# Kernel tuning notes

Measured on AMD Instinct MI355X. Metric: run time of the kernel, lower is better.

Reference implementation:

```python
import jax, jax.numpy as jnp
import numpy as np

B, S, D, H = 2, 2048, 1024, 16
HD = D // H

def setup_inputs() -> dict:
    key = jax.random.key(0)
    ks = jax.random.split(key, 11)
    s = 1.0 / np.sqrt(D)
    return {
        "query": jax.random.normal(ks[0], (B, S, D), jnp.float32),
        "key": jax.random.normal(ks[1], (B, S, D), jnp.float32),
        "value": jax.random.normal(ks[2], (B, S, D), jnp.float32),
        "Wq": jax.random.normal(ks[3], (D, D), jnp.float32) * s,
        "bq": jax.random.normal(ks[4], (D,), jnp.float32) * s,
        "Wk": jax.random.normal(ks[5], (D, D), jnp.float32) * s,
        "bk": jax.random.normal(ks[6], (D,), jnp.float32) * s,
        "Wv": jax.random.normal(ks[7], (D, D), jnp.float32) * s,
        "bv": jax.random.normal(ks[8], (D,), jnp.float32) * s,
        "Wo": jax.random.normal(ks[9], (D, D), jnp.float32) * s,
        "bo": jax.random.normal(ks[10], (D,), jnp.float32) * s,
        "test": 0,
    }

def _heads(x, W, b):
    # [B,S,D] @ [D,D] -> [B,S,D] -> [B,H,S,HD]
    y = x @ W + b
    return y.reshape(B, -1, H, HD).transpose(0, 2, 1, 3)

def reference(query, key, value, Wq, bq, Wk, bk, Wv, bv, Wo, bo, test):
    q = _heads(query, Wq, bq)
    k = _heads(key, Wk, bk)
    v = _heads(value, Wv, bv)
    scale = 1.0 / np.sqrt(HD).astype(np.float32)
    scores = jnp.einsum('bhqd,bhkd->bhqk', q, k) * scale  # [B,H,S,S]
    if test:
        return scores
    prob = jax.nn.softmax(scores, axis=-1)
    out = jnp.einsum('bhqk,bhkd->bhqd', prob, v)
    out = out.transpose(0, 2, 1, 3).reshape(B, -1, D)
    return out @ Wo + bo
```

## Files before the change

kernel.cpp:

```cpp
#include <hip/hip_runtime.h>

constexpr int Bn  = 2;
constexpr int Sn  = 2048;
constexpr int Dn  = 1024;
constexpr int Hn  = 16;
constexpr int HDn = 64;
constexpr int Mn  = Bn * Sn;

typedef _Float16 half8 __attribute__((ext_vector_type(8)));
typedef _Float16 half4 __attribute__((ext_vector_type(4)));
typedef float    f32x4 __attribute__((ext_vector_type(4)));

__device__ __forceinline__ void cp16(const _Float16* g, _Float16* l) {
  __builtin_amdgcn_global_load_lds(
      (__attribute__((address_space(1))) void*)g,
      (__attribute__((address_space(3))) void*)l, 16, 0, 0);
}

__global__ __launch_bounds__(256) void prep_kernel(
    const float* __restrict__ q, const float* __restrict__ k,
    const float* __restrict__ v,
    const float* __restrict__ Wq, const float* __restrict__ Wk,
    const float* __restrict__ Wv, const float* __restrict__ Wo,
    _Float16* __restrict__ Xh, _Float16* __restrict__ WT) {
  __shared__ float tile[64][65];
  const int n = blockIdx.x;
  const int tid = threadIdx.x;
  if (n < 12288) {
    const int z = n >> 12;
    const float* src = (z == 0) ? q : (z == 1) ? k : v;
    _Float16* dst = Xh + (size_t)z * (Mn * Dn);
    int i = (n & 4095) * 256 + tid;
    float4 v4 = ((const float4*)src)[i];
    half4 h;
    h.x = (_Float16)v4.x; h.y = (_Float16)v4.y;
    h.z = (_Float16)v4.z; h.w = (_Float16)v4.w;
    *(half4*)(dst + (size_t)i * 4) = h;
  } else {
    const int m = n - 12288;
    const int z = m >> 8, rem = m & 255;
    const float* W = (z == 0) ? Wq : (z == 1) ? Wk : (z == 2) ? Wv : Wo;
    _Float16* T = WT + (size_t)z * Dn * Dn;
    const int k0 = (rem >> 4) * 64, n0 = (rem & 15) * 64;
#pragma unroll
    for (int i = 0; i < 4; i++) {
      int s = tid + i * 256;
      int r = s >> 4, c4 = s & 15;
      float4 w4 = *(const float4*)(W + (size_t)(k0 + r) * Dn + n0 + c4 * 4);
      tile[r][c4 * 4 + 0] = w4.x; tile[r][c4 * 4 + 1] = w4.y;
      tile[r][c4 * 4 + 2] = w4.z; tile[r][c4 * 4 + 3] = w4.w;
    }
    __syncthreads();
#pragma unroll
    for (int i = 0; i < 2; i++) {
      int s = tid + i * 256;
      int nn = s >> 3, r8 = (s & 7) * 8;
      half8 h;
#pragma unroll
      for (int j = 0; j < 8; j++) h[j] = (_Float16)tile[r8 + j][nn];
      *(half8*)(T + (size_t)(n0 + nn) * Dn + k0 + r8) = h;
    }
  }
}

__global__ __launch_bounds__(256) void proj_kernel(
    const _Float16* __restrict__ Xh, const _Float16* __restrict__ WT,
    const float* __restrict__ bq, const float* __restrict__ bk,
    const float* __restrict__ bv,
    _Float16* __restrict__ Qh, _Float16* __restrict__ Kh,
    _Float16* __restrict__ VT) {
  const int z = blockIdx.z;
  const _Float16* A  = Xh + (size_t)z * Mn * Dn;
  const _Float16* Bm = WT + (size_t)z * Dn * Dn;
  const float* bias = (z == 0) ? bq : (z == 1) ? bk : bv;

  __shared__ __align__(16) _Float16 smem[2 * 128 * 64];
  _Float16* As = smem;
  _Float16* Bs = smem + 128 * 64;

  const int tid  = threadIdx.x;
  const int lane = tid & 63;
  const int w    = tid >> 6;
  const int wm   = (w >> 1) * 64;
  const int wn   = (w & 1) * 64;
  const int m0   = blockIdx.y * 128;
  const int n0   = blockIdx.x * 128;
  const int qd   = lane >> 4;
  const int lm   = lane & 15;

  const int st_r = tid >> 3;
  const int st_u = (tid & 7) ^ (st_r & 7);

  f32x4 acc[4][4];
#pragma unroll
  for (int i = 0; i < 4; i++)
#pragma unroll
    for (int j = 0; j < 4; j++) acc[i][j] = {0.f, 0.f, 0.f, 0.f};

  for (int k0 = 0; k0 < Dn; k0 += 64) {
#pragma unroll
    for (int p = 0; p < 4; p++) {
      int row = st_r + p * 32;
      cp16(A + (size_t)(m0 + row) * Dn + k0 + st_u * 8, As + (tid + p * 256) * 8);
      cp16(Bm + (size_t)(n0 + row) * Dn + k0 + st_u * 8, Bs + (tid + p * 256) * 8);
    }
    __syncthreads();
#pragma unroll
    for (int ks = 0; ks < 2; ks++) {
      const int up = ((ks * 4 + qd) ^ (lm & 7)) * 8;
      half8 a[4], bb[4];
#pragma unroll
      for (int mi = 0; mi < 4; mi++)
        a[mi] = *(const half8*)(As + (wm + mi * 16 + lm) * 64 + up);
#pragma unroll
      for (int ni = 0; ni < 4; ni++)
        bb[ni] = *(const half8*)(Bs + (wn + ni * 16 + lm) * 64 + up);
      if (z < 2) {
#pragma unroll
        for (int mi = 0; mi < 4; mi++)
#pragma unroll
          for (int ni = 0; ni < 4; ni++)
            acc[mi][ni] = __builtin_amdgcn_mfma_f32_16x16x32_f16(bb[ni], a[mi], acc[mi][ni], 0, 0, 0);
      } else {
#pragma unroll
        for (int mi = 0; mi < 4; mi++)
#pragma unroll
          for (int ni = 0; ni < 4; ni++)
            acc[mi][ni] = __builtin_amdgcn_mfma_f32_16x16x32_f16(a[mi], bb[ni], acc[mi][ni], 0, 0, 0);
      }
    }
    __syncthreads();
  }

  char* T = (char*)smem;
  const int b_ = m0 >> 11, s0 = m0 & (Sn - 1), h0 = n0 >> 6;

  if (z < 2) {
    _Float16* out = (z == 0) ? Qh : Kh;
    const float scl = (z == 0) ? 0.125f * 1.44269504089f : 1.0f;
#pragma unroll
    for (int mi = 0; mi < 4; mi++) {
      int tok = wm + mi * 16 + lm;
#pragma unroll
      for (int ni = 0; ni < 4; ni++) {
        int feat = wn + ni * 16 + qd * 4;
        float4 b4 = *(const float4*)(bias + n0 + feat);
        half4 h4;
        h4[0] = (_Float16)((acc[mi][ni][0] + b4.x) * scl);
        h4[1] = (_Float16)((acc[mi][ni][1] + b4.y) * scl);
        h4[2] = (_Float16)((acc[mi][ni][2] + b4.z) * scl);
        h4[3] = (_Float16)((acc[mi][ni][3] + b4.w) * scl);
        *(half4*)(T + tok * 256 + ((feat * 2) ^ ((tok & 7) << 4))) = h4;
      }
    }
    __syncthreads();
#pragma unroll
    for (int i = 0; i < 8; i++) {
      int slot = tid + i * 256;
      int r = slot >> 3, c16 = slot & 7;
      int hh = r >> 7, sm = r & 127;
      half8 v8 = *(const half8*)(T + sm * 256 + ((hh * 128 + c16 * 16) ^ ((sm & 7) << 4)));
      *(half8*)(out + (((size_t)(b_ * Hn + h0 + hh)) * Sn + s0 + sm) * HDn + c16 * 8) = v8;
    }
  } else {
#pragma unroll
    for (int ni = 0; ni < 4; ni++) {
      int feat = wn + ni * 16 + lm;
      float b_f = bias[n0 + feat];
#pragma unroll
      for (int mi = 0; mi < 4; mi++) {
        int tk = wm + mi * 16 + qd * 4;
        half4 h4;
#pragma unroll
        for (int r = 0; r < 4; r++) h4[r] = (_Float16)(acc[mi][ni][r] + b_f);
        *(half4*)(T + feat * 256 + ((tk * 2) ^ ((feat & 7) << 4))) = h4;
      }
    }
    __syncthreads();
#pragma unroll
    for (int i = 0; i < 8; i++) {
      int slot = tid + i * 256;
      int f = slot >> 4, c16 = slot & 15;
      half8 v8 = *(const half8*)(T + f * 256 + ((c16 * 16) ^ ((f & 7) << 4)));
      int head = h0 + (f >> 6), hd = f & 63;
      *(half8*)(VT + (((size_t)(b_ * Hn + head)) * HDn + hd) * Sn + s0 + c16 * 8) = v8;
    }
  }
}

__global__ __launch_bounds__(256, 2) void attn_kernel(
    const _Float16* __restrict__ Qh, const _Float16* __restrict__ Kh,
    const _Float16* __restrict__ VT, _Float16* __restrict__ attn_out) {
  constexpr int PV_LD = 72;
  __shared__ __align__(16) _Float16 Ksb[2][128 * 64];
  __shared__ __align__(16) _Float16 Ps[4 * 32 * PV_LD];

  const int n    = blockIdx.x;
  const int slot = n >> 3;
  const int bh   = (n & 7) * 4 + (slot >> 4);
  const int q0   = (slot & 15) * 128;
  const size_t base = (size_t)bh * Sn * HDn;

  const int tid  = threadIdx.x;
  const int lane = tid & 63;
  const int w    = tid >> 6;
  const int qd   = lane >> 4;
  const int lm   = lane & 15;

  const _Float16* qptr = Qh + base + (size_t)(q0 + w * 32 + lm) * HDn + qd * 8;
  half8 qa[2][2];
#pragma unroll
  for (int nj = 0; nj < 2; nj++)
#pragma unroll
    for (int ks = 0; ks < 2; ks++)
      qa[nj][ks] = *(const half8*)(qptr + nj * 16 * HDn + ks * 32);

  half8 vones;
#pragma unroll
  for (int j = 0; j < 8; j++) vones[j] = (lm == 0) ? (_Float16)1.0f : (_Float16)0.0f;

  f32x4 oacc[2][4];
#pragma unroll
  for (int i = 0; i < 2; i++)
#pragma unroll
    for (int j = 0; j < 4; j++) oacc[i][j] = {0.f, 0.f, 0.f, 0.f};
  f32x4 oaccl[2] = {{0.f, 0.f, 0.f, 0.f}, {0.f, 0.f, 0.f, 0.f}};

  _Float16* Psw = Ps + w * (32 * PV_LD);
  const f32x4 sinit = {-10.f, -10.f, -10.f, -10.f};

  const int st_r = tid >> 3;
  const int st_u = (tid & 7) ^ (st_r & 7);
  const _Float16* kbase = Kh + base;
  const _Float16* vrow  = VT + base + (size_t)lm * Sn + qd * 8;

#define STAGE_K(KT, DST)                                                     \
  {                                                                          \
    const _Float16* src_ = kbase + (size_t)(KT) * 128 * HDn;                 \
    _Float16* dst_ = (DST);                                                  \
    _Pragma("unroll")                                                        \
    for (int p = 0; p < 4; p++)                                              \
      cp16(src_ + (size_t)(st_r + p * 32) * HDn + st_u * 8,                  \
           dst_ + (tid + p * 256) * 8);                                      \
  }

#define LOAD_V(C, VB)                                                        \
  _Pragma("unroll")                                                          \
  for (int oi = 0; oi < 4; oi++)                                             \
    _Pragma("unroll")                                                        \
    for (int k2 = 0; k2 < 2; k2++)                                           \
      VB[oi][k2] = *(const half8*)(vrow + (size_t)(oi * 16) * Sn             \
                                   + kb + (C) * 64 + k2 * 32);

#define QK(C, SACC)                                                          \
  {                                                                          \
    _Pragma("unroll")                                                        \
    for (int n4 = 0; n4 < 4; n4++)                                           \
      _Pragma("unroll")                                                      \
      for (int nj = 0; nj < 2; nj++) SACC[n4][nj] = sinit;                   \
    __builtin_amdgcn_s_setprio(1);                                           \
    _Pragma("unroll")                                                        \
    for (int n4 = 0; n4 < 4; n4++) {                                         \
      int ni = 4 * (C) + n4;                                                 \
      _Pragma("unroll")                                                      \
      for (int ks = 0; ks < 2; ks++) {                                       \
        int up = (4 * ks + qd) ^ (lm & 7);                                   \
        half8 ka = *(const half8*)(Ksb[cur] + (ni * 16 + lm) * HDn + up * 8);\
        _Pragma("unroll")                                                    \
        for (int nj = 0; nj < 2; nj++)                                       \
          SACC[n4][nj] = __builtin_amdgcn_mfma_f32_16x16x32_f16(             \
              ka, qa[nj][ks], SACC[n4][nj], 0, 0, 0);                        \
      }                                                                      \
    }                                                                        \
    __builtin_amdgcn_s_setprio(0);                                           \
  }

#define SM(SACC)                                                             \
  _Pragma("unroll")                                                          \
  for (int nj = 0; nj < 2; nj++)                                             \
    _Pragma("unroll")                                                        \
    for (int n4 = 0; n4 < 4; n4++) {                                         \
      float p0 = __builtin_amdgcn_exp2f(SACC[n4][nj][0]);                    \
      float p1 = __builtin_amdgcn_exp2f(SACC[n4][nj][1]);                    \
      float p2 = __builtin_amdgcn_exp2f(SACC[n4][nj][2]);                    \
      float p3 = __builtin_amdgcn_exp2f(SACC[n4][nj][3]);                    \
      auto lo = __builtin_amdgcn_cvt_pkrtz(p0, p1);                          \
      auto hi = __builtin_amdgcn_cvt_pkrtz(p2, p3);                          \
      half4 h4;                                                              \
      h4[0] = (_Float16)lo[0]; h4[1] = (_Float16)lo[1];                      \
      h4[2] = (_Float16)hi[0]; h4[3] = (_Float16)hi[1];                      \
      *(half4*)(Psw + (nj * 16 + lm) * PV_LD + n4 * 16 + qd * 4) = h4;       \
    }

#define PV(VB)                                                               \
  _Pragma("unroll")                                                          \
  for (int k2 = 0; k2 < 2; k2++) {                                           \
    half8 pa[2];                                                             \
    _Pragma("unroll")                                                        \
    for (int mi = 0; mi < 2; mi++)                                           \
      pa[mi] = *(const half8*)(Psw + (mi * 16 + lm) * PV_LD + k2 * 32 + qd * 8);\
    __builtin_amdgcn_s_setprio(1);                                           \
    _Pragma("unroll")                                                        \
    for (int oi = 0; oi < 4; oi++)                                           \
      _Pragma("unroll")                                                      \
      for (int mi = 0; mi < 2; mi++)                                         \
        oacc[mi][oi] = __builtin_amdgcn_mfma_f32_16x16x32_f16(               \
            VB[oi][k2], pa[mi], oacc[mi][oi], 0, 0, 0);                      \
    _Pragma("unroll")                                                        \
    for (int mi = 0; mi < 2; mi++)                                           \
      oaccl[mi] = __builtin_amdgcn_mfma_f32_16x16x32_f16(                    \
          vones, pa[mi], oaccl[mi], 0, 0, 0);                                \
    __builtin_amdgcn_s_setprio(0);                                           \
  }

  STAGE_K(0, Ksb[0])
  __syncthreads();

  int cur = 0;
  for (int kt = 0; kt < Sn / 128; kt++) {
    const int kb = kt * 128;
    if (kt + 1 < Sn / 128) STAGE_K(kt + 1, Ksb[cur ^ 1])

    f32x4 sacc[2][4][2];
    half8 vbA[4][2], vbB[4][2];

    LOAD_V(0, vbA)
    QK(0, sacc[0])
    QK(1, sacc[1])
    SM(sacc[0])
    LOAD_V(1, vbB)
    PV(vbA)
    SM(sacc[1])
    PV(vbB)

    __syncthreads();
    cur ^= 1;
  }
#undef STAGE_K
#undef LOAD_V
#undef QK
#undef SM
#undef PV

  const int b_ = bh >> 4, h_ = bh & 15;
#pragma unroll
  for (int mi = 0; mi < 2; mi++) {
    float lr = __shfl(oaccl[mi][0], lm, 64);
    float inv = 1.0f / lr;
    int qrow = q0 + w * 32 + mi * 16 + lm;
    size_t rowbase = ((size_t)(b_ * Sn + qrow)) * Dn + h_ * 64;
#pragma unroll
    for (int oi = 0; oi < 4; oi++) {
      half4 h4;
#pragma unroll
      for (int r = 0; r < 4; r++) h4[r] = (_Float16)(oacc[mi][oi][r] * inv);
      *(half4*)(attn_out + rowbase + oi * 16 + qd * 4) = h4;
    }
  }
}

__global__ __launch_bounds__(256) void outproj_kernel(
    const _Float16* __restrict__ Aattn, const _Float16* __restrict__ WoT,
    const float* __restrict__ bo, float* __restrict__ out) {
  __shared__ __align__(16) _Float16 smem[(64 + 128) * 128];
  _Float16* As = smem;
  _Float16* Bs = smem + 64 * 128;

  const int tid  = threadIdx.x;
  const int lane = tid & 63;
  const int w    = tid >> 6;
  const int wm   = (w >> 1) * 32;
  const int wn   = (w & 1) * 64;
  const int m0   = blockIdx.y * 64;
  const int n0   = blockIdx.x * 128;
  const int qd   = lane >> 4;
  const int lm   = lane & 15;

  f32x4 acc[2][4];
#pragma unroll
  for (int i = 0; i < 2; i++)
#pragma unroll
    for (int j = 0; j < 4; j++) acc[i][j] = {0.f, 0.f, 0.f, 0.f};

  for (int k0 = 0; k0 < Dn; k0 += 128) {
#pragma unroll
    for (int p = 0; p < 4; p++) {
      int s = tid + p * 256;
      int r = s >> 4, u = (s & 15) ^ (r & 15);
      cp16(Aattn + (size_t)(m0 + r) * Dn + k0 + u * 8, As + s * 8);
    }
#pragma unroll
    for (int p = 0; p < 8; p++) {
      int s = tid + p * 256;
      int r = s >> 4, u = (s & 15) ^ (r & 15);
      cp16(WoT + (size_t)(n0 + r) * Dn + k0 + u * 8, Bs + s * 8);
    }
    __syncthreads();
#pragma unroll
    for (int ks = 0; ks < 4; ks++) {
      const int up = (ks * 4 + qd) ^ lm;
      half8 a[2], bb[4];
#pragma unroll
      for (int mi = 0; mi < 2; mi++)
        a[mi] = *(const half8*)(As + ((wm + mi * 16 + lm) * 16 + up) * 8);
#pragma unroll
      for (int ni = 0; ni < 4; ni++)
        bb[ni] = *(const half8*)(Bs + ((wn + ni * 16 + lm) * 16 + up) * 8);
#pragma unroll
      for (int mi = 0; mi < 2; mi++)
#pragma unroll
        for (int ni = 0; ni < 4; ni++)
          acc[mi][ni] = __builtin_amdgcn_mfma_f32_16x16x32_f16(bb[ni], a[mi], acc[mi][ni], 0, 0, 0);
    }
    __syncthreads();
  }

  float* T = (float*)smem;
#pragma unroll
  for (int mi = 0; mi < 2; mi++) {
    int m = wm + mi * 16 + lm;
#pragma unroll
    for (int ni = 0; ni < 4; ni++) {
      int nb = wn + ni * 16 + qd * 4;
      float4 b4 = *(const float4*)(bo + n0 + nb);
      f32x4 o;
      o[0] = acc[mi][ni][0] + b4.x;
      o[1] = acc[mi][ni][1] + b4.y;
      o[2] = acc[mi][ni][2] + b4.z;
      o[3] = acc[mi][ni][3] + b4.w;
      *(f32x4*)((char*)T + m * 512 + ((nb * 4) ^ ((m & 7) << 4))) = o;
    }
  }
  __syncthreads();
#pragma unroll
  for (int i = 0; i < 8; i++) {
    int s = tid + i * 256;
    int r = s >> 5, c = s & 31;
    f32x4 v = *(const f32x4*)((char*)T + r * 512 + ((c * 16) ^ ((r & 7) << 4)));
    *(f32x4*)(out + (size_t)(m0 + r) * Dn + n0 + c * 4) = v;
  }
}

extern "C" void kernel_launch(void* const* d_in, const int* in_sizes, int n_in,
                              void* d_out, int out_size, void* d_ws, size_t ws_size,
                              hipStream_t stream) {
  const float* query = (const float*)d_in[0];
  const float* key_  = (const float*)d_in[1];
  const float* value = (const float*)d_in[2];
  const float* Wq = (const float*)d_in[3];
  const float* bq = (const float*)d_in[4];
  const float* Wk = (const float*)d_in[5];
  const float* bk = (const float*)d_in[6];
  const float* Wv = (const float*)d_in[7];
  const float* bv = (const float*)d_in[8];
  const float* Wo = (const float*)d_in[9];
  const float* bo = (const float*)d_in[10];

  _Float16* Xh = (_Float16*)d_ws;
  _Float16* WT = Xh + (size_t)3 * Mn * Dn;
  _Float16* Qh = WT + (size_t)4 * Dn * Dn;
  _Float16* Kh = Qh + (size_t)Mn * Dn;
  _Float16* VT = Kh + (size_t)Mn * Dn;
  _Float16* attnb = Xh;
  float* out = (float*)d_out;

  dim3 blk(256);
  prep_kernel<<<dim3(12288 + 1024), blk, 0, stream>>>(
      query, key_, value, Wq, Wk, Wv, Wo, Xh, WT);
  proj_kernel<<<dim3(Dn / 128, Mn / 128, 3), blk, 0, stream>>>(
      Xh, WT, bq, bk, bv, Qh, Kh, VT);
  attn_kernel<<<dim3(512), blk, 0, stream>>>(Qh, Kh, VT, attnb);
  outproj_kernel<<<dim3(Dn / 128, Mn / 64), blk, 0, stream>>>(
      attnb, WT + (size_t)3 * Dn * Dn, bo, out);
}
```

Baseline: 241.4 us.

## Stage V tiles through double-buffered LDS and XOR-swizzle the P buffer

V fragments were previously read directly from global memory by each wave. They are now copied asynchronously into a double-buffered, XOR-swizzled LDS tile alongside K, and the fragments are read from LDS. The padded P scratch buffer is replaced with an unpadded, XOR-swizzled layout to avoid bank conflicts while saving LDS. This raises LDS use per block (from about 50KB to about 82KB), which may limit the two-blocks-per-CU occupancy target and adds LDS read traffic.

```diff
diff --git a/kernel.cpp b/kernel.cpp
--- a/kernel.cpp
+++ b/kernel.cpp
@@ -191,9 +191,9 @@
 __global__ __launch_bounds__(256, 2) void attn_kernel(
     const _Float16* __restrict__ Qh, const _Float16* __restrict__ Kh,
     const _Float16* __restrict__ VT, _Float16* __restrict__ attn_out) {
-  constexpr int PV_LD = 72;
   __shared__ __align__(16) _Float16 Ksb[2][128 * 64];
-  __shared__ __align__(16) _Float16 Ps[4 * 32 * PV_LD];
+  __shared__ __align__(16) _Float16 Vsb[2][64 * 128];
+  __shared__ __align__(16) _Float16 Ps[4 * 32 * 64];
 
   const int n    = blockIdx.x;
   const int slot = n >> 3;
@@ -226,13 +226,13 @@
     for (int j = 0; j < 4; j++) oacc[i][j] = {0.f, 0.f, 0.f, 0.f};
   f32x4 oaccl[2] = {{0.f, 0.f, 0.f, 0.f}, {0.f, 0.f, 0.f, 0.f}};
 
-  _Float16* Psw = Ps + w * (32 * PV_LD);
+  char* Psw = (char*)(Ps + w * (32 * 64));
   const f32x4 sinit = {-10.f, -10.f, -10.f, -10.f};
 
   const int st_r = tid >> 3;
   const int st_u = (tid & 7) ^ (st_r & 7);
   const _Float16* kbase = Kh + base;
-  const _Float16* vrow  = VT + base + (size_t)lm * Sn + qd * 8;
+  const _Float16* vbase = VT + base;
 
 #define STAGE_K(KT, DST)                                                     \
   {                                                                          \
@@ -244,13 +244,24 @@
            dst_ + (tid + p * 256) * 8);                                      \
   }
 
+#define STAGE_V(KT, DST)                                                     \
+  {                                                                          \
+    _Float16* dst_ = (DST);                                                  \
+    _Pragma("unroll")                                                        \
+    for (int p = 0; p < 4; p++) {                                            \
+      int s_ = tid + p * 256;                                                \
+      int r_ = s_ >> 4, u_ = (s_ & 15) ^ (r_ & 15);                          \
+      cp16(vbase + (size_t)r_ * Sn + (KT) * 128 + u_ * 8, dst_ + s_ * 8);    \
+    }                                                                        \
+  }
+
 #define LOAD_V(C, VB)                                                        \
   _Pragma("unroll")                                                          \
   for (int oi = 0; oi < 4; oi++)                                             \
     _Pragma("unroll")                                                        \
     for (int k2 = 0; k2 < 2; k2++)                                           \
-      VB[oi][k2] = *(const half8*)(vrow + (size_t)(oi * 16) * Sn             \
-                                   + kb + (C) * 64 + k2 * 32);
+      VB[oi][k2] = *(const half8*)(Vsb[cur] +                                \
+          ((oi * 16 + lm) * 16 + (((C) * 8 + k2 * 4 + qd) ^ lm)) * 8);
 
 #define QK(C, SACC)                                                          \
   {                                                                          \
@@ -289,7 +300,8 @@
       half4 h4;                                                              \
       h4[0] = (_Float16)lo[0]; h4[1] = (_Float16)lo[1];                      \
       h4[2] = (_Float16)hi[0]; h4[3] = (_Float16)hi[1];                      \
-      *(half4*)(Psw + (nj * 16 + lm) * PV_LD + n4 * 16 + qd * 4) = h4;       \
+      *(half4*)(Psw + (nj * 16 + lm) * 128 +                                 \
+                ((n4 * 32 + qd * 8) ^ ((lm & 7) << 4))) = h4;                \
     }
 
 #define PV(VB)                                                               \
@@ -298,7 +310,8 @@
     half8 pa[2];                                                             \
     _Pragma("unroll")                                                        \
     for (int mi = 0; mi < 2; mi++)                                           \
-      pa[mi] = *(const half8*)(Psw + (mi * 16 + lm) * PV_LD + k2 * 32 + qd * 8);\
+      pa[mi] = *(const half8*)(Psw + (mi * 16 + lm) * 128 +                  \
+                               ((k2 * 64 + qd * 16) ^ ((lm & 7) << 4)));     \
     __builtin_amdgcn_s_setprio(1);                                           \
     _Pragma("unroll")                                                        \
     for (int oi = 0; oi < 4; oi++)                                           \
@@ -314,12 +327,15 @@
   }
 
   STAGE_K(0, Ksb[0])
+  STAGE_V(0, Vsb[0])
   __syncthreads();
 
   int cur = 0;
   for (int kt = 0; kt < Sn / 128; kt++) {
-    const int kb = kt * 128;
-    if (kt + 1 < Sn / 128) STAGE_K(kt + 1, Ksb[cur ^ 1])
+    if (kt + 1 < Sn / 128) {
+      STAGE_K(kt + 1, Ksb[cur ^ 1])
+      STAGE_V(kt + 1, Vsb[cur ^ 1])
+    }
 
     f32x4 sacc[2][4][2];
     half8 vbA[4][2], vbB[4][2];
@@ -337,6 +353,7 @@
     cur ^= 1;
   }
 #undef STAGE_K
+#undef STAGE_V
 #undef LOAD_V
 #undef QK
 #undef SM
```

New measurement: 224.7 us, median of 2. 1.07x faster.
